# Kernel optimization log

Measured on AMD Instinct MI355X. Metric: run time of the kernel, lower is better.

The kernel has to match this reference:

```python
import jax, jax.numpy as jnp
import numpy as np

B, S, D, H = 4, 2048, 1024, 16
DK = D // H

def setup_inputs() -> dict:
    key = jax.random.key(0)
    ks = jax.random.split(key, 5)
    std = np.sqrt(2.0 / (D + D)).astype(np.float32)
    return {
        "x": jax.random.normal(ks[0], (B, S, D), dtype=jnp.float32),
        "W_q": jax.random.normal(ks[1], (D, D), dtype=jnp.float32) * std,
        "W_k": jax.random.normal(ks[2], (D, D), dtype=jnp.float32) * std,
        "W_v": jax.random.normal(ks[3], (D, D), dtype=jnp.float32) * std,
        "W_o": jax.random.normal(ks[4], (D, D), dtype=jnp.float32) * std,
    }

def reference(x, W_q, W_k, W_v, W_o):
    b, s, d = x.shape
    # Linear layers: y = x @ W.T  (W stored as [out, in])
    q = (x @ W_q.T).reshape(b, s, H, DK).transpose(0, 2, 1, 3)  # [b,h,s,dk]
    k = (x @ W_k.T).reshape(b, s, H, DK).transpose(0, 2, 1, 3)
    v = (x @ W_v.T).reshape(b, s, H, DK).transpose(0, 2, 1, 3)
    scale = 1.0 / jnp.sqrt(jnp.asarray(DK, dtype=x.dtype))
    scores = jnp.einsum("bhqd,bhkd->bhqk", q, k) * scale  # [b,h,s,s]
    causal = jnp.tril(jnp.ones((s, s), dtype=bool))
    scores = jnp.where(causal, scores, jnp.asarray(-jnp.inf, dtype=scores.dtype))
    attn = jax.nn.softmax(scores, axis=-1)
    out = jnp.einsum("bhqk,bhkd->bhqd", attn, v)  # [b,h,s,dk]
    out = out.transpose(0, 2, 1, 3).reshape(b, s, d)
    return out @ W_o.T
```

## Files before the change

kernel.cpp:

```cpp
#include <hip/hip_runtime.h>
#include <stdint.h>

#define B_  4
#define S_  2048
#define D_  1024
#define H_  16
#define DK_ 64
#define M_  (B_ * S_)

typedef __attribute__((ext_vector_type(4))) float  f32x4;
typedef __attribute__((ext_vector_type(8))) __bf16 bf16x8;
typedef __attribute__((ext_vector_type(4))) unsigned short us4;

__device__ __forceinline__ unsigned short cvt_bf16(float f) {
  unsigned u = __float_as_uint(f);
  return (unsigned short)((u + 0x7fffu + ((u >> 16) & 1u)) >> 16);
}

__device__ __forceinline__ f32x4 mfma16(bf16x8 a, bf16x8 b, f32x4 c) {
  return __builtin_amdgcn_mfma_f32_16x16x32_bf16(a, b, c, 0, 0, 0);
}

__device__ __forceinline__ void async16(const void* g, void* l) {
  __builtin_amdgcn_global_load_lds(
      (const __attribute__((address_space(1))) void*)g,
      (__attribute__((address_space(3))) void*)l, 16, 0, 0);
}

#define XN4_ 2097152
#define WN4_ 262144
__global__ void cast_all(const float* __restrict__ x,
                         const float* __restrict__ wq,
                         const float* __restrict__ wk,
                         const float* __restrict__ wv,
                         const float* __restrict__ wo,
                         unsigned short* __restrict__ dst) {
  const int i = blockIdx.x * blockDim.x + threadIdx.x;
  const float* src;
  int k;
  if (i < XN4_) {
    src = x; k = i;
  } else {
    const int j = i - XN4_;
    const int wsel = j >> 18;
    k = j & (WN4_ - 1);
    src = (wsel == 0) ? wq : (wsel == 1) ? wk : (wsel == 2) ? wv : wo;
  }
  f32x4 v = ((const f32x4*)src)[k];
  us4 o;
  o[0] = cvt_bf16(v[0]); o[1] = cvt_bf16(v[1]);
  o[2] = cvt_bf16(v[2]); o[3] = cvt_bf16(v[3]);
  ((us4*)dst)[i] = o;
}

template <int OUTMODE>
__global__ __launch_bounds__(256) void gemm_bt(
    const unsigned short* __restrict__ A,
    const unsigned short* __restrict__ Bm,
    void* __restrict__ Cp,
    unsigned short* __restrict__ Qo, unsigned short* __restrict__ Ko,
    unsigned short* __restrict__ Vto,
    int Ndim, int Kdim) {
  constexpr int BM = 128, BN = 128, BK = 64;
  __shared__ __align__(16) unsigned short As[BM * BK];
  __shared__ __align__(16) unsigned short Bs[BN * BK];

  const int tid = threadIdx.x;
  const int w = tid >> 6, l = tid & 63;
  const int l16 = l & 15, lg = l >> 4;
  const int wr = w >> 1, wc = w & 1;
  const int rowA0 = blockIdx.y * BM;
  const int rowB0 = blockIdx.x * BN;

  f32x4 acc[4][4] = {};

  for (int kt = 0; kt < Kdim; kt += BK) {
#pragma unroll
    for (int j = 0; j < 4; ++j) {
      const int ci = j * 256 + w * 64;
      const int i  = ci + l;
      const int r  = i >> 3;
      const int cc = (i & 7) ^ (r & 7);
      async16(A  + (size_t)(rowA0 + r) * Kdim + kt + cc * 8, &As[ci * 8]);
      async16(Bm + (size_t)(rowB0 + r) * Kdim + kt + cc * 8, &Bs[ci * 8]);
    }
    __syncthreads();
#pragma unroll
    for (int hf = 0; hf < 2; ++hf) {
      bf16x8 af[4], bfr[4];
#pragma unroll
      for (int m = 0; m < 4; ++m) {
        const int r = wr * 64 + m * 16 + l16;
        const int byte = (r * 128) + ((lg * 16 + hf * 64) ^ ((r & 7) << 4));
        af[m] = *(const bf16x8*)((const char*)As + byte);
      }
#pragma unroll
      for (int n = 0; n < 4; ++n) {
        const int r = wc * 64 + n * 16 + l16;
        const int byte = (r * 128) + ((lg * 16 + hf * 64) ^ ((r & 7) << 4));
        bfr[n] = *(const bf16x8*)((const char*)Bs + byte);
      }
#pragma unroll
      for (int m = 0; m < 4; ++m)
#pragma unroll
        for (int n = 0; n < 4; ++n)
          acc[m][n] = mfma16(af[m], bfr[n], acc[m][n]);
    }
    __syncthreads();
  }

  const int rb = rowA0 + wr * 64;
  const int cb = rowB0 + wc * 64;
  if constexpr (OUTMODE == 2) {
    float* C = (float*)Cp;
#pragma unroll
    for (int m = 0; m < 4; ++m)
#pragma unroll
      for (int n = 0; n < 4; ++n) {
        const int r0 = rb + m * 16 + lg * 4;
        const int c0 = cb + n * 16 + l16;
#pragma unroll
        for (int j = 0; j < 4; ++j)
          C[(size_t)(r0 + j) * Ndim + c0] = acc[m][n][j];
      }
  } else {
    const int region = cb >> 10;
    const int cbl = cb & 1023;
    if (region < 2) {
      unsigned short* C = region ? Ko : Qo;
#pragma unroll
      for (int m = 0; m < 4; ++m)
#pragma unroll
        for (int n = 0; n < 4; ++n) {
          const int r0 = rb + m * 16 + lg * 4;
          const int c0 = cbl + n * 16 + l16;
#pragma unroll
          for (int j = 0; j < 4; ++j)
            C[(size_t)(r0 + j) * 1024 + c0] = cvt_bf16(acc[m][n][j]);
        }
    } else {
#pragma unroll
      for (int m = 0; m < 4; ++m)
#pragma unroll
        for (int n = 0; n < 4; ++n) {
          const int r0 = rb + m * 16 + lg * 4;
          const int c0 = cbl + n * 16 + l16;
          us4 v;
#pragma unroll
          for (int j = 0; j < 4; ++j) v[j] = cvt_bf16(acc[m][n][j]);
          *(us4*)&Vto[((size_t)(r0 >> 11) * 1024 + c0) * 2048 + (r0 & 2047)] = v;
        }
    }
  }
}


#define SMX(sc, mr, sr, oa, P, diag, rb, kv0)                                \
  do {                                                                       \
    _Pragma("unroll") for (int nc_ = 0; nc_ < 4; ++nc_)                      \
        _Pragma("unroll") for (int j_ = 0; j_ < 4; ++j_)                     \
            sc[nc_][j_] *= 0.125f;                                           \
    if (diag) {                                                              \
      _Pragma("unroll") for (int nc_ = 0; nc_ < 4; ++nc_) {                  \
        const int col_ = (kv0) + nc_ * 16 + l16;                             \
        _Pragma("unroll") for (int j_ = 0; j_ < 4; ++j_)                     \
            if (col_ > (rb) + j_) sc[nc_][j_] = -INFINITY;                   \
      }                                                                      \
    }                                                                        \
    _Pragma("unroll") for (int j_ = 0; j_ < 4; ++j_) {                       \
      float t_ = fmaxf(fmaxf(sc[0][j_], sc[1][j_]),                          \
                       fmaxf(sc[2][j_], sc[3][j_]));                         \
      t_ = fmaxf(t_, __shfl_xor(t_, 1));                                     \
      t_ = fmaxf(t_, __shfl_xor(t_, 2));                                     \
      t_ = fmaxf(t_, __shfl_xor(t_, 4));                                     \
      t_ = fmaxf(t_, __shfl_xor(t_, 8));                                     \
      const float mnew_ = fmaxf(mr[j_], t_);                                 \
      float rs_ = 0.f;                                                       \
      _Pragma("unroll") for (int nc_ = 0; nc_ < 4; ++nc_) {                  \
        const float p_ = __expf(sc[nc_][j_] - mnew_);                        \
        rs_ += p_;                                                           \
        P[lg * 4 + j_][nc_ * 16 + l16] = cvt_bf16(p_);                       \
      }                                                                      \
      rs_ += __shfl_xor(rs_, 1);                                             \
      rs_ += __shfl_xor(rs_, 2);                                             \
      rs_ += __shfl_xor(rs_, 4);                                             \
      rs_ += __shfl_xor(rs_, 8);                                             \
      const float al_ = __expf(mr[j_] - mnew_);                              \
      sr[j_] = sr[j_] * al_ + rs_;                                           \
      mr[j_] = mnew_;                                                        \
      _Pragma("unroll") for (int d_ = 0; d_ < 4; ++d_) oa[d_][j_] *= al_;    \
    }                                                                        \
  } while (0)

__global__ __launch_bounds__(256, 4) void flash_attn(
    const unsigned short* __restrict__ Q,
    const unsigned short* __restrict__ K,
    const unsigned short* __restrict__ Vt,
    unsigned short* __restrict__ O) {
  const int bid  = blockIdx.x;
  const int virt = (bid & 7) * 128 + (bid >> 3);
  const int bh   = virt >> 4;
  const int x    = virt & 15;
  const int b = bh >> 4, h = bh & 15;
  const int tid = threadIdx.x;
  const int w = tid >> 6, l = tid & 63;
  const int l16 = l & 15, lg = l >> 4;

  __shared__ __align__(16) unsigned short Ks[64 * 64];
  __shared__ __align__(16) unsigned short Vs[64 * 64];
  __shared__ __align__(16) unsigned short PA[4][16][72];
  __shared__ __align__(16) unsigned short PB[4][16][72];

  const int tA = x, tB = 31 - x;

  const size_t qkbase = (size_t)(b * S_) * D_ + h * DK_;
  const size_t vbase  = ((size_t)(b * D_) + h * DK_) * S_;

  const int rA = tA * 64 + w * 16 + l16;
  const int rB = tB * 64 + w * 16 + l16;
  bf16x8 qfA[2], qfB[2];
  qfA[0] = *(const bf16x8*)&Q[qkbase + (size_t)rA * D_ + lg * 8];
  qfA[1] = *(const bf16x8*)&Q[qkbase + (size_t)rA * D_ + 32 + lg * 8];
  qfB[0] = *(const bf16x8*)&Q[qkbase + (size_t)rB * D_ + lg * 8];
  qfB[1] = *(const bf16x8*)&Q[qkbase + (size_t)rB * D_ + 32 + lg * 8];

  float mA[4], sA[4], mB[4], sB[4];
  f32x4 oA[4] = {}, oB[4] = {};
#pragma unroll
  for (int j = 0; j < 4; ++j) {
    mA[j] = mB[j] = -INFINITY;
    sA[j] = sB[j] = 0.f;
  }

  const int rbA = tA * 64 + w * 16 + lg * 4;
  const int rbB = tB * 64 + w * 16 + lg * 4;

  for (int kv = 0; kv <= tB; ++kv) {
    const int kv0 = kv * 64;
    if (kv) __syncthreads();
#pragma unroll
    for (int c = 0; c < 2; ++c) {
      const int ci = c * 256 + w * 64;
      const int i  = ci + l;
      const int r  = i >> 3;
      const int cc = (i & 7) ^ (r & 7);
      async16(K  + qkbase + (size_t)(kv0 + r) * D_ + cc * 8, &Ks[ci * 8]);
      async16(Vt + vbase  + (size_t)r * S_ + kv0 + cc * 8,   &Vs[ci * 8]);
    }
    __syncthreads();

    if (kv <= tA) {
      f32x4 sc[4] = {};
#pragma unroll
      for (int nc = 0; nc < 4; ++nc) {
        const int r = nc * 16 + l16;
#pragma unroll
        for (int ks = 0; ks < 2; ++ks) {
          const int byte = (r * 128 + ks * 64 + lg * 16) ^ ((r & 7) << 4);
          bf16x8 kf = *(const bf16x8*)((const char*)Ks + byte);
          sc[nc] = mfma16(qfA[ks], kf, sc[nc]);
        }
      }
      SMX(sc, mA, sA, oA, PA[w], kv == tA, rbA, kv0);
      __asm__ volatile("s_waitcnt lgkmcnt(0)" ::: "memory");
      bf16x8 pa0 = *(const bf16x8*)&PA[w][l16][lg * 8];
      bf16x8 pa1 = *(const bf16x8*)&PA[w][l16][32 + lg * 8];
#pragma unroll
      for (int d = 0; d < 4; ++d) {
        const int r = d * 16 + l16;
#pragma unroll
        for (int ks = 0; ks < 2; ++ks) {
          const int byte = (r * 128 + ks * 64 + lg * 16) ^ ((r & 7) << 4);
          bf16x8 vf = *(const bf16x8*)((const char*)Vs + byte);
          oA[d] = mfma16(ks ? pa1 : pa0, vf, oA[d]);
        }
      }
    }

    {
      f32x4 sc[4] = {};
#pragma unroll
      for (int nc = 0; nc < 4; ++nc) {
        const int r = nc * 16 + l16;
#pragma unroll
        for (int ks = 0; ks < 2; ++ks) {
          const int byte = (r * 128 + ks * 64 + lg * 16) ^ ((r & 7) << 4);
          bf16x8 kf = *(const bf16x8*)((const char*)Ks + byte);
          sc[nc] = mfma16(qfB[ks], kf, sc[nc]);
        }
      }
      SMX(sc, mB, sB, oB, PB[w], kv == tB, rbB, kv0);
      __asm__ volatile("s_waitcnt lgkmcnt(0)" ::: "memory");
      bf16x8 pb0 = *(const bf16x8*)&PB[w][l16][lg * 8];
      bf16x8 pb1 = *(const bf16x8*)&PB[w][l16][32 + lg * 8];
#pragma unroll
      for (int d = 0; d < 4; ++d) {
        const int r = d * 16 + l16;
#pragma unroll
        for (int ks = 0; ks < 2; ++ks) {
          const int byte = (r * 128 + ks * 64 + lg * 16) ^ ((r & 7) << 4);
          bf16x8 vf = *(const bf16x8*)((const char*)Vs + byte);
          oB[d] = mfma16(ks ? pb1 : pb0, vf, oB[d]);
        }
      }
    }
  }

#pragma unroll
  for (int d = 0; d < 4; ++d)
#pragma unroll
    for (int j = 0; j < 4; ++j) {
      O[((size_t)(b * S_) + rbA + j) * D_ + h * DK_ + d * 16 + l16] =
          cvt_bf16(oA[d][j] / sA[j]);
      O[((size_t)(b * S_) + rbB + j) * D_ + h * DK_ + d * 16 + l16] =
          cvt_bf16(oB[d][j] / sB[j]);
    }
}

extern "C" void kernel_launch(void* const* d_in, const int* in_sizes, int n_in,
                              void* d_out, int out_size, void* d_ws,
                              size_t ws_size, hipStream_t stream) {
  const float* x  = (const float*)d_in[0];
  const float* Wq = (const float*)d_in[1];
  const float* Wk = (const float*)d_in[2];
  const float* Wv = (const float*)d_in[3];
  const float* Wo = (const float*)d_in[4];

  const size_t XN = (size_t)M_ * D_;
  const size_t WN = (size_t)D_ * D_;
  unsigned short* xb  = (unsigned short*)d_ws;
  unsigned short* Wqb = xb + XN;
  unsigned short* Wob = Wqb + 3 * WN;
  unsigned short* Qb  = Wob + WN;
  unsigned short* Kb  = Qb + XN;
  unsigned short* Vtb = Kb + XN;
  unsigned short* Ob  = Vtb + XN;

  cast_all<<<(XN4_ + 4 * WN4_) / 256, 256, 0, stream>>>(x, Wq, Wk, Wv, Wo, xb);

  gemm_bt<3><<<dim3(24, 64), 256, 0, stream>>>(xb, Wqb, nullptr, Qb, Kb, Vtb,
                                               3072, D_);

  flash_attn<<<dim3(1024), 256, 0, stream>>>(Qb, Kb, Vtb, Ob);

  gemm_bt<2><<<dim3(8, 64), 256, 0, stream>>>(Ob, Wob, d_out, nullptr, nullptr,
                                              nullptr, D_, D_);
}
```

Measured before the change: 304.9 us.

## Double-buffer K/V tiles in flash attention and remap GEMM blocks per XCD

The attention kernel now keeps two LDS buffers for K and V and issues the async load of the next KV tile before computing on the current one. This lets the global-to-LDS transfer overlap the MFMA and softmax work, and it leaves one barrier per iteration. Both GEMM launches switch to a 1D grid whose block index is remapped so that consecutive tiles land on the same XCD, with the goal of better L2 reuse. The cost is twice the K/V LDS per block, which may reduce occupancy under launch_bounds(256,4).

```diff
diff --git a/kernel.cpp b/kernel.cpp
--- a/kernel.cpp
+++ b/kernel.cpp
@@ -60,17 +60,24 @@
     void* __restrict__ Cp,
     unsigned short* __restrict__ Qo, unsigned short* __restrict__ Ko,
     unsigned short* __restrict__ Vto,
-    int Ndim, int Kdim) {
+    int gx, int Ndim, int Kdim) {
   constexpr int BM = 128, BN = 128, BK = 64;
   __shared__ __align__(16) unsigned short As[BM * BK];
   __shared__ __align__(16) unsigned short Bs[BN * BK];
+
+  const int nwg = gridDim.x;
+  const int cpx = nwg >> 3;
+  const int bid = blockIdx.x;
+  const int virt = (bid & 7) * cpx + (bid >> 3);
+  const int bx = virt % gx;
+  const int by = virt / gx;
 
   const int tid = threadIdx.x;
   const int w = tid >> 6, l = tid & 63;
   const int l16 = l & 15, lg = l >> 4;
   const int wr = w >> 1, wc = w & 1;
-  const int rowA0 = blockIdx.y * BM;
-  const int rowB0 = blockIdx.x * BN;
+  const int rowA0 = by * BM;
+  const int rowB0 = bx * BN;
 
   f32x4 acc[4][4] = {};
 
@@ -192,6 +199,21 @@
     }                                                                        \
   } while (0)
 
+#define STAGE(kvt, pb)                                                       \
+  do {                                                                       \
+    const int kv0_ = (kvt) * 64;                                             \
+    _Pragma("unroll") for (int c_ = 0; c_ < 2; ++c_) {                       \
+      const int ci_ = c_ * 256 + w * 64;                                     \
+      const int i_  = ci_ + l;                                               \
+      const int r_  = i_ >> 3;                                               \
+      const int cc_ = (i_ & 7) ^ (r_ & 7);                                   \
+      async16(K  + qkbase + (size_t)(kv0_ + r_) * D_ + cc_ * 8,              \
+              &Ks[pb][ci_ * 8]);                                             \
+      async16(Vt + vbase  + (size_t)r_ * S_ + kv0_ + cc_ * 8,                \
+              &Vs[pb][ci_ * 8]);                                             \
+    }                                                                        \
+  } while (0)
+
 __global__ __launch_bounds__(256, 4) void flash_attn(
     const unsigned short* __restrict__ Q,
     const unsigned short* __restrict__ K,
@@ -206,8 +228,8 @@
   const int w = tid >> 6, l = tid & 63;
   const int l16 = l & 15, lg = l >> 4;
 
-  __shared__ __align__(16) unsigned short Ks[64 * 64];
-  __shared__ __align__(16) unsigned short Vs[64 * 64];
+  __shared__ __align__(16) unsigned short Ks[2][64 * 64];
+  __shared__ __align__(16) unsigned short Vs[2][64 * 64];
   __shared__ __align__(16) unsigned short PA[4][16][72];
   __shared__ __align__(16) unsigned short PB[4][16][72];
 
@@ -235,19 +257,16 @@
   const int rbA = tA * 64 + w * 16 + lg * 4;
   const int rbB = tB * 64 + w * 16 + lg * 4;
 
+  STAGE(0, 0);
+  __syncthreads();
+
   for (int kv = 0; kv <= tB; ++kv) {
+    const int p = kv & 1;
     const int kv0 = kv * 64;
-    if (kv) __syncthreads();
-#pragma unroll
-    for (int c = 0; c < 2; ++c) {
-      const int ci = c * 256 + w * 64;
-      const int i  = ci + l;
-      const int r  = i >> 3;
-      const int cc = (i & 7) ^ (r & 7);
-      async16(K  + qkbase + (size_t)(kv0 + r) * D_ + cc * 8, &Ks[ci * 8]);
-      async16(Vt + vbase  + (size_t)r * S_ + kv0 + cc * 8,   &Vs[ci * 8]);
-    }
-    __syncthreads();
+    if (kv < tB) STAGE(kv + 1, p ^ 1);
+
+    const char* Kp = (const char*)&Ks[p][0];
+    const char* Vp = (const char*)&Vs[p][0];
 
     if (kv <= tA) {
       f32x4 sc[4] = {};
@@ -257,7 +276,7 @@
 #pragma unroll
         for (int ks = 0; ks < 2; ++ks) {
           const int byte = (r * 128 + ks * 64 + lg * 16) ^ ((r & 7) << 4);
-          bf16x8 kf = *(const bf16x8*)((const char*)Ks + byte);
+          bf16x8 kf = *(const bf16x8*)(Kp + byte);
           sc[nc] = mfma16(qfA[ks], kf, sc[nc]);
         }
       }
@@ -271,7 +290,7 @@
 #pragma unroll
         for (int ks = 0; ks < 2; ++ks) {
           const int byte = (r * 128 + ks * 64 + lg * 16) ^ ((r & 7) << 4);
-          bf16x8 vf = *(const bf16x8*)((const char*)Vs + byte);
+          bf16x8 vf = *(const bf16x8*)(Vp + byte);
           oA[d] = mfma16(ks ? pa1 : pa0, vf, oA[d]);
         }
       }
@@ -285,7 +304,7 @@
 #pragma unroll
         for (int ks = 0; ks < 2; ++ks) {
           const int byte = (r * 128 + ks * 64 + lg * 16) ^ ((r & 7) << 4);
-          bf16x8 kf = *(const bf16x8*)((const char*)Ks + byte);
+          bf16x8 kf = *(const bf16x8*)(Kp + byte);
           sc[nc] = mfma16(qfB[ks], kf, sc[nc]);
         }
       }
@@ -299,11 +318,12 @@
 #pragma unroll
         for (int ks = 0; ks < 2; ++ks) {
           const int byte = (r * 128 + ks * 64 + lg * 16) ^ ((r & 7) << 4);
-          bf16x8 vf = *(const bf16x8*)((const char*)Vs + byte);
+          bf16x8 vf = *(const bf16x8*)(Vp + byte);
           oB[d] = mfma16(ks ? pb1 : pb0, vf, oB[d]);
         }
       }
     }
+    __syncthreads();
   }
 
 #pragma unroll
@@ -338,11 +358,11 @@
 
   cast_all<<<(XN4_ + 4 * WN4_) / 256, 256, 0, stream>>>(x, Wq, Wk, Wv, Wo, xb);
 
-  gemm_bt<3><<<dim3(24, 64), 256, 0, stream>>>(xb, Wqb, nullptr, Qb, Kb, Vtb,
-                                               3072, D_);
+  gemm_bt<3><<<1536, 256, 0, stream>>>(xb, Wqb, nullptr, Qb, Kb, Vtb,
+                                       24, 3072, D_);
 
   flash_attn<<<dim3(1024), 256, 0, stream>>>(Qb, Kb, Vtb, Ob);
 
-  gemm_bt<2><<<dim3(8, 64), 256, 0, stream>>>(Ob, Wob, d_out, nullptr, nullptr,
-                                              nullptr, D_, D_);
-}
+  gemm_bt<2><<<512, 256, 0, stream>>>(Ob, Wob, d_out, nullptr, nullptr,
+                                      nullptr, 8, D_, D_);
+}
```

Measured after the change: 320.7 us. 1.05x slower.
